# Kernel optimization log

Measured on AMD Instinct MI355X. Metric: run time of the kernel, lower is better.

## Reference

```python
import jax, jax.numpy as jnp
import numpy as np

EMBED = 1024
HEADS = 16
HEAD_DIM = EMBED // HEADS
NEG = -1e20


def setup_inputs() -> dict:
    key = jax.random.key(0)
    ks = jax.random.split(key, 8)
    N, S = 2, 2048
    values = jax.random.normal(ks[0], (N, S, EMBED), dtype=jnp.float32)
    keys = jax.random.normal(ks[1], (N, S, EMBED), dtype=jnp.float32)
    queries = jax.random.normal(ks[2], (N, S, EMBED), dtype=jnp.float32)
    mask = jnp.ones((N, 1, 1, S), dtype=jnp.int32)
    s = 1.0 / np.sqrt(HEAD_DIM)
    Wv = jax.random.normal(ks[3], (HEAD_DIM, HEAD_DIM), dtype=jnp.float32) * s
    Wk = jax.random.normal(ks[4], (HEAD_DIM, HEAD_DIM), dtype=jnp.float32) * s
    Wq = jax.random.normal(ks[5], (HEAD_DIM, HEAD_DIM), dtype=jnp.float32) * s
    Wo = jax.random.normal(ks[6], (EMBED, EMBED), dtype=jnp.float32) * (1.0 / np.sqrt(EMBED))
    bo = jnp.zeros((EMBED,), dtype=jnp.float32)
    return {"values": values, "keys": keys, "queries": queries, "mask": mask,
            "Wv": Wv, "Wk": Wk, "Wq": Wq, "Wo": Wo, "bo": bo}


def reference(values, keys, queries, mask, Wv, Wk, Wq, Wo, bo):
    N, q_len, E = queries.shape
    v_len, k_len = values.shape[1], keys.shape[1]
    H, D = HEADS, HEAD_DIM
    # split heads: [N, L, H, D]
    v = values.reshape(N, v_len, H, D)
    k = keys.reshape(N, k_len, H, D)
    q = queries.reshape(N, q_len, H, D)
    # per-head linear projections (shared across heads), torch Linear: x @ W.T
    v = jnp.einsum('nlhd,ed->nlhe', v, Wv)
    k = jnp.einsum('nlhd,ed->nlhe', k, Wk)
    q = jnp.einsum('nlhd,ed->nlhe', q, Wq)
    # scores [N, H, q, k]
    scores = jnp.einsum('nqhd,nkhd->nhqk', q, k)
    scores = jnp.where(mask == 0, NEG, scores)
    # NOTE: original scales by sqrt(embed_size), not sqrt(head_dim)
    attn = jax.nn.softmax(scores / (E ** 0.5), axis=3)
    out = jnp.einsum('nhqk,nkhd->nqhd', attn, v).reshape(N, q_len, E)
    return out @ Wo.T + bo
```

## Files before the change

kernel.cpp:

```cpp
#include <hip/hip_runtime.h>

typedef __bf16 bf16_t;
typedef __bf16 bf16x8 __attribute__((ext_vector_type(8)));
typedef __bf16 bf16x4 __attribute__((ext_vector_type(4)));
typedef float f32x4 __attribute__((ext_vector_type(4)));
typedef float f32x16 __attribute__((ext_vector_type(16)));

#define MFMA16(a, b, c) __builtin_amdgcn_mfma_f32_16x16x32_bf16((a), (b), (c), 0, 0, 0)
#define MFMA32(a, b, c) __builtin_amdgcn_mfma_f32_32x32x16_bf16((a), (b), (c), 0, 0, 0)

namespace {
constexpr int S_LEN = 2048;
constexpr int EMB   = 1024;
constexpr int HEADS = 16;
constexpr int HD    = 64;
constexpr float Q_PRESCALE = 1.44269504088896340736f / 32.0f;
constexpr float NEG_L2     = -4.5084e18f;
}

__device__ __forceinline__ bf16x8 load8_cvt(const float* __restrict__ p) {
    const f32x4 a = *(const f32x4*)p;
    const f32x4 b = *(const f32x4*)(p + 4);
    bf16x8 r;
    r[0] = (bf16_t)a[0]; r[1] = (bf16_t)a[1]; r[2] = (bf16_t)a[2]; r[3] = (bf16_t)a[3];
    r[4] = (bf16_t)b[0]; r[5] = (bf16_t)b[1]; r[6] = (bf16_t)b[2]; r[7] = (bf16_t)b[3];
    return r;
}

__device__ __forceinline__ unsigned pk_bf16(float lo, float hi) {
    union { bf16_t h[2]; unsigned u; } u;
    u.h[0] = (bf16_t)lo; u.h[1] = (bf16_t)hi;
    return u.u;
}

__global__ __launch_bounds__(256) void proj_kernel(
    const float* __restrict__ values, const float* __restrict__ keys,
    const float* __restrict__ queries,
    const float* __restrict__ Wv, const float* __restrict__ Wk,
    const float* __restrict__ Wq,
    bf16_t* __restrict__ Qp, bf16_t* __restrict__ Kf, bf16_t* __restrict__ Vf)
{
    const int tid = threadIdx.x;
    const int w = tid >> 6, l = tid & 63, g = l >> 4, q15 = l & 15;
    const int b   = blockIdx.x;
    const int mat = b >> 10;
    const int rem = b & 1023;
    const int h   = rem >> 6;
    const int t0  = (((rem & 63) << 2) + w) << 4;
    const int n   = t0 >> 11;
    const int s0  = t0 & 2047;

    if (mat < 2) {
        const float* X = (mat == 0) ? queries : keys;
        const float* W = (mat == 0) ? Wq : Wk;
        const float scl = (mat == 0) ? Q_PRESCALE : 1.0f;
        const float* xr = X + (size_t)(t0 + q15) * EMB + h * HD + g * 8;
        bf16x8 a0 = load8_cvt(xr);
        bf16x8 a1 = load8_cvt(xr + 32);
        f32x4 acc[4];
        #pragma unroll
        for (int nt = 0; nt < 4; ++nt) acc[nt] = (f32x4){0.f, 0.f, 0.f, 0.f};
        #pragma unroll
        for (int nt = 0; nt < 4; ++nt) {
            const float* wr = W + (nt * 16 + q15) * HD + g * 8;
            bf16x8 b0 = load8_cvt(wr);
            bf16x8 b1 = load8_cvt(wr + 32);
            acc[nt] = MFMA16(a0, b0, acc[nt]);
            acc[nt] = MFMA16(a1, b1, acc[nt]);
        }
        if (mat == 0) {
            bf16_t* O = Qp + (size_t)(n * HEADS + h) * S_LEN * HD;
            #pragma unroll
            for (int nt = 0; nt < 4; ++nt)
                #pragma unroll
                for (int r = 0; r < 4; ++r)
                    O[(size_t)(s0 + g * 4 + r) * HD + nt * 16 + q15] = (bf16_t)(acc[nt][r] * scl);
        } else {
            bf16_t* O = Kf + (size_t)(n * HEADS + h) * S_LEN * HD;
            const int ktb  = s0 >> 5;
            const int lrow = s0 & 31;
            const int hi8  = (q15 >> 3) * 256 + (q15 & 7);
            #pragma unroll
            for (int nt = 0; nt < 4; ++nt)
                #pragma unroll
                for (int r = 0; r < 4; ++r)
                    O[(size_t)(ktb * 4 + nt) * 512 + hi8 + (lrow + g * 4 + r) * 8]
                        = (bf16_t)acc[nt][r];
        }
    } else {
        const float* xr = values + (size_t)(t0 + q15) * EMB + h * HD + g * 8;
        bf16x8 b0 = load8_cvt(xr);
        bf16x8 b1 = load8_cvt(xr + 32);
        bf16_t* O = Vf + (size_t)(n * HEADS + h) * S_LEN * HD;
        f32x4 acc[4];
        #pragma unroll
        for (int et = 0; et < 4; ++et) acc[et] = (f32x4){0.f, 0.f, 0.f, 0.f};
        #pragma unroll
        for (int et = 0; et < 4; ++et) {
            const float* wr = Wv + (et * 16 + q15) * HD + g * 8;
            bf16x8 a0 = load8_cvt(wr);
            bf16x8 a1 = load8_cvt(wr + 32);
            acc[et] = MFMA16(a0, b0, acc[et]);
            acc[et] = MFMA16(a1, b1, acc[et]);
        }
        const int kt2 = (s0 >> 6) * 2;
        const int ksl = (s0 >> 4) & 3;
        const int hi8 = (q15 >> 3) * 256 + (q15 & 7);
        #pragma unroll
        for (int et = 0; et < 4; ++et)
            #pragma unroll
            for (int r = 0; r < 4; ++r)
                O[(size_t)((kt2 + (et >> 1)) * 4 + ksl) * 512 + hi8
                  + ((et & 1) * 16 + g * 4 + r) * 8] = (bf16_t)acc[et][r];
    }
}

template<int SPLIT>
__global__ __launch_bounds__(256, 2) void attn_kernel(
    const bf16_t* __restrict__ Qp, const bf16_t* __restrict__ Kf,
    const bf16_t* __restrict__ Vf, const int* __restrict__ mask,
    bf16_t* __restrict__ Out, float* __restrict__ Lp)
{
    __shared__ bf16_t plds[4][32][72];
    const int tid = threadIdx.x;
    const int w = tid >> 6, l = tid & 63;
    const int l31 = l & 31, hi = l >> 5;
    const int bid = blockIdx.x;
    const int half = (SPLIT == 2) ? (bid >> 9) : 0;
    const int rem  = bid & 511;
    const int nh = rem & 31, qt = rem >> 5;
    const int n = nh >> 4, h = nh & 15;
    const size_t hb = (size_t)nh * S_LEN * HD;
    const int qb = qt * 128 + w * 32;
    const int kt0 = half * (32 / SPLIT);
    const int ktN = kt0 + 32 / SPLIT;

    bf16x8 qf[4];
    {
        const bf16_t* qr = Qp + hb + (size_t)(qb + l31) * HD + hi * 8;
        #pragma unroll
        for (int d = 0; d < 4; ++d) qf[d] = *(const bf16x8*)(qr + d * 16);
    }

    const int* __restrict__ mrow = mask + n * S_LEN;
    const bf16_t* kp0 = Kf + hb + (size_t)l * 8;
    const bf16_t* vp0 = Vf + hb + (size_t)l * 8;

    bool anyZero = false;
    {
        const int* mp = mrow + (l >> 1) * 64 + (l & 1) * 32;
        #pragma unroll
        for (int j = 0; j < 8; ++j) {
            const int4 mv = *(const int4*)(mp + 4 * j);
            anyZero |= (mv.x == 0) | (mv.y == 0) | (mv.z == 0) | (mv.w == 0);
        }
    }
    const unsigned long long maskbal = __ballot(anyZero);

    f32x16 acc0, acc1;
    #pragma unroll
    for (int i = 0; i < 16; ++i) { acc0[i] = 0.f; acc1[i] = 0.f; }
    float l_run = 0.0f;

    bf16x8 kbuf0[8], kbuf1[8];
    auto loadK = [&](bf16x8* buf, int kt_) {
        const bf16_t* p = kp0 + (size_t)(kt_ * 8) * 512;
        #pragma unroll
        for (int j = 0; j < 8; ++j) buf[j] = *(const bf16x8*)(p + j * 512);
    };

    auto tile = [&](int kt, bf16x8* kf, bf16x8* nkf, bool pref) {
        bf16x8 vf[8];
        {
            const bf16_t* p = vp0 + (size_t)(kt * 8) * 512;
            #pragma unroll
            for (int j = 0; j < 8; ++j) vf[j] = *(const bf16x8*)(p + j * 512);
        }

        f32x16 s0, s1;
        #pragma unroll
        for (int i = 0; i < 16; ++i) { s0[i] = 0.f; s1[i] = 0.f; }
        #pragma unroll
        for (int d = 0; d < 4; ++d) s0 = MFMA32(kf[d],     qf[d], s0);
        #pragma unroll
        for (int d = 0; d < 4; ++d) s1 = MFMA32(kf[4 + d], qf[d], s1);

        if (pref) loadK(nkf, kt + 1);

        if ((maskbal >> (2 * kt)) & 3ull) {
            const unsigned long long mb = __ballot(mrow[kt * 64 + l] != 0);
            #pragma unroll
            for (int r = 0; r < 16; ++r) {
                const int cr = (r & 3) + 8 * (r >> 2) + 4 * hi;
                if (!((mb >> cr) & 1ull))        s0[r] = NEG_L2;
                if (!((mb >> (32 + cr)) & 1ull)) s1[r] = NEG_L2;
            }
        }

        float ts0 = 0.f, ts1 = 0.f;
        #pragma unroll
        for (int r = 0; r < 16; ++r) {
            const float p0 = exp2f(s0[r]);
            const float p1 = exp2f(s1[r]);
            s0[r] = p0; s1[r] = p1;
            ts0 += p0; ts1 += p1;
        }
        l_run += ts0 + ts1;

        union U8 { unsigned u[4]; bf16x8 v; };
        bf16x8 pa[4];
        #pragma unroll
        for (int b = 0; b < 2; ++b) {
            #pragma unroll
            for (int t = 0; t < 2; ++t) {
                const int rb = t * 8;
                float e0, e1, e2, e3, e4, e5, e6, e7;
                if (b == 0) {
                    e0 = s0[rb]; e1 = s0[rb + 1]; e2 = s0[rb + 2]; e3 = s0[rb + 3];
                    e4 = s0[rb + 4]; e5 = s0[rb + 5]; e6 = s0[rb + 6]; e7 = s0[rb + 7];
                } else {
                    e0 = s1[rb]; e1 = s1[rb + 1]; e2 = s1[rb + 2]; e3 = s1[rb + 3];
                    e4 = s1[rb + 4]; e5 = s1[rb + 5]; e6 = s1[rb + 6]; e7 = s1[rb + 7];
                }
                const unsigned a01 = pk_bf16(e0, e1);
                const unsigned a23 = pk_bf16(e2, e3);
                const unsigned b01 = pk_bf16(e4, e5);
                const unsigned b23 = pk_bf16(e6, e7);
                const unsigned y1 = hi ? a01 : b01;
                const unsigned y2 = hi ? a23 : b23;
                const unsigned r1 = (unsigned)__shfl_xor((int)y1, 32);
                const unsigned r2 = (unsigned)__shfl_xor((int)y2, 32);
                U8 f;
                f.u[0] = hi ? r1 : a01;
                f.u[1] = hi ? r2 : a23;
                f.u[2] = hi ? b01 : r1;
                f.u[3] = hi ? b23 : r2;
                pa[2 * b + t] = f.v;
            }
        }

        #pragma unroll
        for (int ksl = 0; ksl < 4; ++ksl) {
            acc0 = MFMA32(pa[ksl], vf[ksl],     acc0);
            acc1 = MFMA32(pa[ksl], vf[4 + ksl], acc1);
        }
    };

    loadK(kbuf0, kt0);
    for (int kt = kt0; kt < ktN; kt += 2) {
        tile(kt,     kbuf0, kbuf1, true);
        tile(kt + 1, kbuf1, kbuf0, kt + 1 < ktN - 1);
    }

    const float l_tot = l_run + __shfl_xor(l_run, 32);
    if (SPLIT == 1) {
        const float inv = 1.0f / l_tot;
        #pragma unroll
        for (int r = 0; r < 16; ++r) {
            const int cr = (r & 3) + 8 * (r >> 2) + 4 * hi;
            const float iq = __shfl(inv, cr);
            plds[w][cr][l31]      = (bf16_t)(acc0[r] * iq);
            plds[w][cr][32 + l31] = (bf16_t)(acc1[r] * iq);
        }
        __syncthreads();
        const int rr = l >> 1, c0 = (l & 1) * 32;
        const bf16x8 o0 = *(const bf16x8*)&plds[w][rr][c0];
        const bf16x8 o1 = *(const bf16x8*)&plds[w][rr][c0 + 8];
        const bf16x8 o2 = *(const bf16x8*)&plds[w][rr][c0 + 16];
        const bf16x8 o3 = *(const bf16x8*)&plds[w][rr][c0 + 24];
        bf16_t* op = Out + (size_t)(n * S_LEN + qb + rr) * EMB + h * HD + c0;
        *(bf16x8*)(op)      = o0;
        *(bf16x8*)(op + 8)  = o1;
        *(bf16x8*)(op + 16) = o2;
        *(bf16x8*)(op + 24) = o3;
    } else {
        #pragma unroll
        for (int r = 0; r < 16; ++r) {
            const int cr = (r & 3) + 8 * (r >> 2) + 4 * hi;
            plds[w][cr][l31]      = (bf16_t)acc0[r];
            plds[w][cr][32 + l31] = (bf16_t)acc1[r];
        }
        if (hi == 0) Lp[(half << 16) + nh * S_LEN + qb + l31] = l_tot;
        __syncthreads();
        const int rr = l >> 1, c0 = (l & 1) * 32;
        const bf16x8 o0 = *(const bf16x8*)&plds[w][rr][c0];
        const bf16x8 o1 = *(const bf16x8*)&plds[w][rr][c0 + 8];
        const bf16x8 o2 = *(const bf16x8*)&plds[w][rr][c0 + 16];
        const bf16x8 o3 = *(const bf16x8*)&plds[w][rr][c0 + 24];
        bf16_t* op = Out + ((size_t)(half * 32 + nh) * S_LEN + qb + rr) * HD + c0;
        *(bf16x8*)(op)      = o0;
        *(bf16x8*)(op + 8)  = o1;
        *(bf16x8*)(op + 16) = o2;
        *(bf16x8*)(op + 24) = o3;
    }
}

__global__ __launch_bounds__(256) void merge_kernel(
    const bf16_t* __restrict__ Opart, const float* __restrict__ Lp,
    bf16_t* __restrict__ AO)
{
    const int gid = blockIdx.x * 256 + threadIdx.x;
    const int gq = gid >> 2, seg = (gid & 3) * 16;
    const int nh = gq >> 11, s = gq & 2047;
    const int n = nh >> 4, h = nh & 15;
    const float inv = 1.0f / (Lp[gq] + Lp[65536 + gq]);
    const bf16_t* p0 = Opart + (size_t)gq * HD + seg;
    const bf16_t* p1 = p0 + (size_t)32 * S_LEN * HD;
    const bf16x8 a0 = *(const bf16x8*)(p0);
    const bf16x8 a1 = *(const bf16x8*)(p0 + 8);
    const bf16x8 b0 = *(const bf16x8*)(p1);
    const bf16x8 b1 = *(const bf16x8*)(p1 + 8);
    bf16x8 r0, r1;
    #pragma unroll
    for (int j = 0; j < 8; ++j) {
        r0[j] = (bf16_t)(((float)a0[j] + (float)b0[j]) * inv);
        r1[j] = (bf16_t)(((float)a1[j] + (float)b1[j]) * inv);
    }
    bf16_t* op = AO + (size_t)(n * S_LEN + s) * EMB + h * HD + seg;
    *(bf16x8*)(op)     = r0;
    *(bf16x8*)(op + 8) = r1;
}

__global__ __launch_bounds__(256) void outproj_kernel(
    const bf16_t* __restrict__ X, const float* __restrict__ Wo,
    const float* __restrict__ bo, float* __restrict__ out)
{
    __shared__ bf16_t Xs[128 * 64];
    __shared__ bf16_t Ws[64 * 64];
    const int tid = threadIdx.x;
    const int w = tid >> 6, l = tid & 63, g = l >> 4, q15 = l & 15;
    const int m0 = (blockIdx.x >> 4) * 128;
    const int n0 = (blockIdx.x & 15) * 64;
    const int wm = (w >> 1) * 64, wn = (w & 1) * 32;

    f32x4 acc[4][2];
    #pragma unroll
    for (int i = 0; i < 4; ++i)
        #pragma unroll
        for (int j = 0; j < 2; ++j) acc[i][j] = (f32x4){0.f, 0.f, 0.f, 0.f};

    for (int k0 = 0; k0 < EMB; k0 += 64) {
        __syncthreads();
        #pragma unroll
        for (int j = 0; j < 4; ++j) {
            const int cid = tid + 256 * j;
            const int r = cid >> 3, pc = cid & 7;
            const int sw = (pc ^ (r & 7)) * 8;
            *(bf16x8*)&Xs[r * 64 + sw] =
                *(const bf16x8*)(X + (size_t)(m0 + r) * EMB + k0 + pc * 8);
        }
        #pragma unroll
        for (int j = 0; j < 2; ++j) {
            const int cid = tid + 256 * j;
            const int r = cid >> 3, pc = cid & 7;
            const int sw = (pc ^ (r & 7)) * 8;
            *(bf16x8*)&Ws[r * 64 + sw] =
                load8_cvt(Wo + (size_t)(n0 + r) * EMB + k0 + pc * 8);
        }
        __syncthreads();
        #pragma unroll
        for (int c = 0; c < 2; ++c) {
            bf16x8 av[4], bv[2];
            #pragma unroll
            for (int mt = 0; mt < 4; ++mt) {
                const int r = wm + mt * 16 + q15;
                av[mt] = *(const bf16x8*)&Xs[r * 64 + (((4 * c + g) ^ (r & 7)) * 8)];
            }
            #pragma unroll
            for (int nt = 0; nt < 2; ++nt) {
                const int r = wn + nt * 16 + q15;
                bv[nt] = *(const bf16x8*)&Ws[r * 64 + (((4 * c + g) ^ (r & 7)) * 8)];
            }
            #pragma unroll
            for (int mt = 0; mt < 4; ++mt)
                #pragma unroll
                for (int nt = 0; nt < 2; ++nt)
                    acc[mt][nt] = MFMA16(av[mt], bv[nt], acc[mt][nt]);
        }
    }

    float bias[2];
    #pragma unroll
    for (int nt = 0; nt < 2; ++nt) bias[nt] = bo[n0 + wn + nt * 16 + q15];
    #pragma unroll
    for (int mt = 0; mt < 4; ++mt)
        #pragma unroll
        for (int nt = 0; nt < 2; ++nt)
            #pragma unroll
            for (int r = 0; r < 4; ++r)
                out[(size_t)(m0 + wm + mt * 16 + g * 4 + r) * EMB + n0 + wn + nt * 16 + q15]
                    = acc[mt][nt][r] + bias[nt];
}

extern "C" void kernel_launch(void* const* d_in, const int* in_sizes, int n_in,
                              void* d_out, int out_size, void* d_ws, size_t ws_size,
                              hipStream_t stream) {
    const float* values  = (const float*)d_in[0];
    const float* keys    = (const float*)d_in[1];
    const float* queries = (const float*)d_in[2];
    const int*   mask    = (const int*)d_in[3];
    const float* Wv      = (const float*)d_in[4];
    const float* Wk      = (const float*)d_in[5];
    const float* Wq      = (const float*)d_in[6];
    const float* Wo      = (const float*)d_in[7];
    const float* bo      = (const float*)d_in[8];
    float* out = (float*)d_out;

    bf16_t* Qp    = (bf16_t*)d_ws;
    bf16_t* Kf    = Qp + (size_t)4194304;
    bf16_t* Vf    = Kf + (size_t)4194304;
    bf16_t* AO    = Vf + (size_t)4194304;
    bf16_t* Opart = AO + (size_t)4194304;
    float*  Lp    = (float*)((char*)d_ws + (size_t)48 * 1024 * 1024);

    proj_kernel<<<3072, 256, 0, stream>>>(values, keys, queries, Wv, Wk, Wq, Qp, Kf, Vf);

    const bool split2 = ws_size >= (size_t)50 * 1024 * 1024;
    if (split2) {
        attn_kernel<2><<<1024, 256, 0, stream>>>(Qp, Kf, Vf, mask, Opart, Lp);
        merge_kernel<<<1024, 256, 0, stream>>>(Opart, Lp, AO);
    } else {
        attn_kernel<1><<<512, 256, 0, stream>>>(Qp, Kf, Vf, mask, AO, nullptr);
    }

    outproj_kernel<<<512, 256, 0, stream>>>(AO, Wo, bo, out);
}
```

Measured before the change: 129.7 us.

## Fuse split-K merge into output projection, raise attention occupancy, use fast exp2

Removes the separate merge kernel. The output projection now reads both partial attention outputs and their row sums directly while staging its X tile, normalising on the fly. This saves one launch and a write and read of the AO intermediate. Separately, attention launch bounds go from 2 to 3 waves per SIMD, and exp2f is swapped for the hardware exp2 builtin. Risks include register spills under the tighter bound and redundant divides per tile load.

After: 250.6 us. 93.2% more time.

```diff
diff --git a/kernel.cpp b/kernel.cpp
--- a/kernel.cpp
+++ b/kernel.cpp
@@ -8,6 +8,7 @@
 
 #define MFMA16(a, b, c) __builtin_amdgcn_mfma_f32_16x16x32_bf16((a), (b), (c), 0, 0, 0)
 #define MFMA32(a, b, c) __builtin_amdgcn_mfma_f32_32x32x16_bf16((a), (b), (c), 0, 0, 0)
+#define EXP2(x) __builtin_amdgcn_exp2f(x)
 
 namespace {
 constexpr int S_LEN = 2048;
@@ -116,7 +117,7 @@
 }
 
 template<int SPLIT>
-__global__ __launch_bounds__(256, 2) void attn_kernel(
+__global__ __launch_bounds__(256, 3) void attn_kernel(
     const bf16_t* __restrict__ Qp, const bf16_t* __restrict__ Kf,
     const bf16_t* __restrict__ Vf, const int* __restrict__ mask,
     bf16_t* __restrict__ Out, float* __restrict__ Lp)
@@ -172,9 +173,9 @@
     auto tile = [&](int kt, bf16x8* kf, bf16x8* nkf, bool pref) {
         bf16x8 vf[8];
         {
-            const bf16_t* p = vp0 + (size_t)(kt * 8) * 512;
-            #pragma unroll
-            for (int j = 0; j < 8; ++j) vf[j] = *(const bf16x8*)(p + j * 512);
+            const bf16_t* pv = vp0 + (size_t)(kt * 8) * 512;
+            #pragma unroll
+            for (int j = 0; j < 8; ++j) vf[j] = *(const bf16x8*)(pv + j * 512);
         }
 
         f32x16 s0, s1;
@@ -200,8 +201,8 @@
         float ts0 = 0.f, ts1 = 0.f;
         #pragma unroll
         for (int r = 0; r < 16; ++r) {
-            const float p0 = exp2f(s0[r]);
-            const float p1 = exp2f(s1[r]);
+            const float p0 = EXP2(s0[r]);
+            const float p1 = EXP2(s1[r]);
             s0[r] = p0; s1[r] = p1;
             ts0 += p0; ts1 += p1;
         }
@@ -295,34 +296,10 @@
     }
 }
 
-__global__ __launch_bounds__(256) void merge_kernel(
-    const bf16_t* __restrict__ Opart, const float* __restrict__ Lp,
-    bf16_t* __restrict__ AO)
-{
-    const int gid = blockIdx.x * 256 + threadIdx.x;
-    const int gq = gid >> 2, seg = (gid & 3) * 16;
-    const int nh = gq >> 11, s = gq & 2047;
-    const int n = nh >> 4, h = nh & 15;
-    const float inv = 1.0f / (Lp[gq] + Lp[65536 + gq]);
-    const bf16_t* p0 = Opart + (size_t)gq * HD + seg;
-    const bf16_t* p1 = p0 + (size_t)32 * S_LEN * HD;
-    const bf16x8 a0 = *(const bf16x8*)(p0);
-    const bf16x8 a1 = *(const bf16x8*)(p0 + 8);
-    const bf16x8 b0 = *(const bf16x8*)(p1);
-    const bf16x8 b1 = *(const bf16x8*)(p1 + 8);
-    bf16x8 r0, r1;
-    #pragma unroll
-    for (int j = 0; j < 8; ++j) {
-        r0[j] = (bf16_t)(((float)a0[j] + (float)b0[j]) * inv);
-        r1[j] = (bf16_t)(((float)a1[j] + (float)b1[j]) * inv);
-    }
-    bf16_t* op = AO + (size_t)(n * S_LEN + s) * EMB + h * HD + seg;
-    *(bf16x8*)(op)     = r0;
-    *(bf16x8*)(op + 8) = r1;
-}
-
+template<int FUSED>
 __global__ __launch_bounds__(256) void outproj_kernel(
-    const bf16_t* __restrict__ X, const float* __restrict__ Wo,
+    const bf16_t* __restrict__ X, const bf16_t* __restrict__ Opart,
+    const float* __restrict__ Lp, const float* __restrict__ Wo,
     const float* __restrict__ bo, float* __restrict__ out)
 {
     __shared__ bf16_t Xs[128 * 64];
@@ -346,8 +323,25 @@
             const int cid = tid + 256 * j;
             const int r = cid >> 3, pc = cid & 7;
             const int sw = (pc ^ (r & 7)) * 8;
-            *(bf16x8*)&Xs[r * 64 + sw] =
-                *(const bf16x8*)(X + (size_t)(m0 + r) * EMB + k0 + pc * 8);
+            if (FUSED) {
+                const int row = m0 + r;
+                const int nn = row >> 11, ss = row & 2047;
+                const int hh = k0 >> 6;
+                const int gq = (nn * HEADS + hh) * S_LEN + ss;
+                const float inv = 1.0f / (Lp[gq] + Lp[65536 + gq]);
+                const bf16_t* p0 = Opart + (size_t)gq * HD + pc * 8;
+                const bf16_t* p1 = p0 + (size_t)32 * S_LEN * HD;
+                const bf16x8 a = *(const bf16x8*)p0;
+                const bf16x8 b = *(const bf16x8*)p1;
+                bf16x8 x;
+                #pragma unroll
+                for (int e = 0; e < 8; ++e)
+                    x[e] = (bf16_t)(((float)a[e] + (float)b[e]) * inv);
+                *(bf16x8*)&Xs[r * 64 + sw] = x;
+            } else {
+                *(bf16x8*)&Xs[r * 64 + sw] =
+                    *(const bf16x8*)(X + (size_t)(m0 + r) * EMB + k0 + pc * 8);
+            }
         }
         #pragma unroll
         for (int j = 0; j < 2; ++j) {
@@ -418,10 +412,9 @@
     const bool split2 = ws_size >= (size_t)50 * 1024 * 1024;
     if (split2) {
         attn_kernel<2><<<1024, 256, 0, stream>>>(Qp, Kf, Vf, mask, Opart, Lp);
-        merge_kernel<<<1024, 256, 0, stream>>>(Opart, Lp, AO);
+        outproj_kernel<1><<<512, 256, 0, stream>>>(nullptr, Opart, Lp, Wo, bo, out);
     } else {
         attn_kernel<1><<<512, 256, 0, stream>>>(Qp, Kf, Vf, mask, AO, nullptr);
-    }
-
-    outproj_kernel<<<512, 256, 0, stream>>>(AO, Wo, bo, out);
-}
+        outproj_kernel<0><<<512, 256, 0, stream>>>(AO, nullptr, nullptr, Wo, bo, out);
+    }
+}
```
